# Kernel optimization log

Hardware: AMD Instinct MI355X
Metric: run time of the kernel (lower is better)

Reference implementation:

```python
import jax, jax.numpy as jnp
import numpy as np

TOP_K = 2


def setup_inputs() -> dict:
    key = jax.random.key(0)
    ks = jax.random.split(key, 6)
    B, S, D, E = 4, 2048, 1024, 8
    d_ff = 4 * D
    x = jax.random.normal(ks[0], (B, S, D), dtype=jnp.float32)
    router_w = jax.random.normal(ks[1], (E, D), dtype=jnp.float32) * 0.02
    w_fc = jax.random.normal(ks[2], (E, d_ff, D), dtype=jnp.float32) * 0.02
    w_proj = jax.random.normal(ks[3], (E, D, d_ff), dtype=jnp.float32) * 0.02
    shared_fc = jax.random.normal(ks[4], (d_ff, D), dtype=jnp.float32) * 0.02
    shared_proj = jax.random.normal(ks[5], (D, d_ff), dtype=jnp.float32) * 0.02
    return {"x": x, "router_w": router_w, "w_fc": w_fc, "w_proj": w_proj,
            "shared_fc": shared_fc, "shared_proj": shared_proj}


def _mlp(x, w_fc, w_proj):
    # c_proj(relu(c_fc(x))^2); torch Linear: y = x @ W.T
    return jnp.square(jax.nn.relu(x @ w_fc.T)) @ w_proj.T


def reference(x, router_w, w_fc, w_proj, shared_fc, shared_proj):
    B, S, D = x.shape
    E = router_w.shape[0]
    T = B * S
    flat = x.reshape(T, D)
    # Router: softmax in fp32, top-k, renormalize
    logits = flat @ router_w.T                                   # [T, E]
    probs = jax.nn.softmax(logits.astype(jnp.float32), axis=-1)
    topk_p, topk_i = jax.lax.top_k(probs, TOP_K)                 # [T, k]
    topk_w = (topk_p / jnp.maximum(topk_p.sum(-1, keepdims=True), 1e-9)).astype(flat.dtype)
    # Dense combine weights [T, E]: scatter normalized top-k weights per token
    combine = jnp.zeros((T, E), dtype=flat.dtype)
    combine = combine.at[jnp.arange(T)[:, None], topk_i].add(topk_w)
    # Expert compute (loop over small fixed E), weighted combine
    out = jnp.zeros_like(flat)
    for e in range(E):
        out = out + _mlp(flat, w_fc[e], w_proj[e]) * combine[:, e:e + 1]
    # Shared expert applied to all tokens
    out = out + _mlp(flat, shared_fc, shared_proj)
    return out.reshape(B, S, D)
```

## Files before the change

kernel.cpp:

```cpp
#include <hip/hip_runtime.h>

#define DEVFN __device__ __forceinline__

typedef _Float16 f16x8 __attribute__((ext_vector_type(8)));
typedef float f32x4 __attribute__((ext_vector_type(4)));

static constexpr int T   = 8192;
static constexpr int D   = 1024;
static constexpr int E   = 8;
static constexpr int DFF = 4096;
static constexpr int NG  = E + 1;
static constexpr int RTOT = 3*T;
static constexpr int MAXRT = (2*T)/128 + E + T/128;

DEVFN unsigned short f2h_bits(float v){
  _Float16 h = (_Float16)v;
  return __builtin_bit_cast(unsigned short, h);
}

DEVFN void gload_lds16(const void* g, void* l){
  __builtin_amdgcn_global_load_lds((const __attribute__((address_space(1))) void*)g,
                                   (__attribute__((address_space(3))) void*)l, 16, 0, 0);
}

__global__ __launch_bounds__(256) void cast_all_kernel(
    const float* __restrict__ s0, const float* __restrict__ s1,
    const float* __restrict__ s2, const float* __restrict__ s3,
    unsigned short* __restrict__ d0, unsigned short* __restrict__ d1,
    unsigned short* __restrict__ d2, unsigned short* __restrict__ d3,
    int n0, int n1, int n2, int n3){
  int total = n0 + n1 + n2 + n3;
  for (int j = blockIdx.x*256 + threadIdx.x; j < total; j += gridDim.x*256){
    const float* sp; unsigned short* dp; int loc = j;
    if (loc < n0){ sp = s0; dp = d0; }
    else if ((loc -= n0) < n1){ sp = s1; dp = d1; }
    else if ((loc -= n1) < n2){ sp = s2; dp = d2; }
    else { loc -= n2; sp = s3; dp = d3; }
    float4 v = ((const float4*)sp)[loc];
    ushort4 o;
    o.x = f2h_bits(v.x); o.y = f2h_bits(v.y); o.z = f2h_bits(v.z); o.w = f2h_bits(v.w);
    ((ushort4*)dp)[loc] = o;
  }
}

__global__ __launch_bounds__(256) void router_kernel(const float* __restrict__ x,
    const float* __restrict__ rw, unsigned short* __restrict__ xb,
    int* __restrict__ tok_e, float* __restrict__ tok_w, int* __restrict__ counts){
  const int lane = threadIdx.x & 63;
  const int t = blockIdx.x*4 + (threadIdx.x >> 6);
  const float4* xp = (const float4*)(x + (size_t)t*D);
  ushort4* xo = (ushort4*)(xb + (size_t)t*D);
  float acc[E];
#pragma unroll
  for (int e=0;e<E;e++) acc[e]=0.f;
#pragma unroll
  for (int i=0;i<4;i++){
    float4 xv = xp[lane + (i<<6)];
    ushort4 o; o.x=f2h_bits(xv.x); o.y=f2h_bits(xv.y); o.z=f2h_bits(xv.z); o.w=f2h_bits(xv.w);
    xo[lane + (i<<6)] = o;
#pragma unroll
    for (int e=0;e<E;e++){
      float4 wv = ((const float4*)(rw + e*D))[lane + (i<<6)];
      acc[e] = fmaf(xv.x,wv.x, fmaf(xv.y,wv.y, fmaf(xv.z,wv.z, fmaf(xv.w,wv.w, acc[e]))));
    }
  }
#pragma unroll
  for (int e=0;e<E;e++){
#pragma unroll
    for (int off=32; off>0; off>>=1) acc[e] += __shfl_xor(acc[e], off);
  }
  if (lane==0){
    float l0=-1e30f, l1=-1e30f; int e0=0, e1=0;
#pragma unroll
    for (int e=0;e<E;e++){
      float v = acc[e];
      if (v > l0){ l1=l0; e1=e0; l0=v; e0=e; }
      else if (v > l1){ l1=v; e1=e; }
    }
    float r   = expf(l1 - l0);
    float inv = 1.f/(1.f + r);
    tok_e[2*t]   = e0; tok_e[2*t+1] = e1;
    tok_w[2*t]   = inv; tok_w[2*t+1] = r*inv;
    atomicAdd(&counts[e0], 1);
    atomicAdd(&counts[e1], 1);
  }
}

__global__ void scan_kernel(const int* __restrict__ counts, int* __restrict__ offs,
                            int* __restrict__ tile_g, int* __restrict__ tile_r0,
                            int* __restrict__ nrt){
  if (blockIdx.x==0 && threadIdx.x==0){
    int off=0, nt=0;
    for (int e=0;e<E;e++){
      offs[e]=off;
      int c = counts[e];
      int tiles = (c+127)>>7;
      for (int i=0;i<tiles;i++){ tile_g[nt]=e; tile_r0[nt]=off + (i<<7); nt++; }
      off += c;
    }
    offs[E] = off;
    for (int i=0;i<T/128;i++){ tile_g[nt]=E; tile_r0[nt]=2*T + (i<<7); nt++; }
    offs[E+1] = 3*T;
    *nrt = nt;
  }
}

__global__ __launch_bounds__(256) void scatter_kernel(const int* __restrict__ tok_e,
    const float* __restrict__ tok_w, const int* __restrict__ offs,
    int* __restrict__ fill, int* __restrict__ row_tok, float* __restrict__ row_w,
    int* __restrict__ inv2){
  int idx = blockIdx.x*256 + threadIdx.x;
  if (idx < 2*T){
    int e = tok_e[idx];
    int pos = offs[e] + atomicAdd(&fill[e], 1);
    row_tok[pos] = idx >> 1;
    row_w[pos]   = tok_w[idx];
    inv2[idx]    = pos;
  } else {
    row_tok[idx] = idx - 2*T;
    row_w[idx]   = 1.0f;
  }
}

template<int MODE>
__global__ __launch_bounds__(256, 2) void gemm8p_kernel(
    const unsigned short* __restrict__ A, const unsigned short* __restrict__ Ball,
    unsigned short* __restrict__ O,
    const int K, const int N, const int CT,
    const int* __restrict__ tile_g, const int* __restrict__ tile_r0,
    const int* __restrict__ offs, const int* __restrict__ nrt,
    const int* __restrict__ row_tok)
{
  const int nwg  = gridDim.x * gridDim.y;
  const int orig = blockIdx.y * gridDim.x + blockIdx.x;
  const int q8 = nwg >> 3, r8 = nwg & 7;
  const int xcd = orig & 7, pos = orig >> 3;
  const int wg = (xcd < r8 ? xcd*(q8+1) : r8*(q8+1) + (xcd-r8)*q8) + pos;
  const int rt = wg / CT, ct = wg - rt*CT;
  if (rt >= *nrt) return;

  const int g    = tile_g[rt];
  const int row0 = tile_r0[rt];
  const int row_end = offs[g+1];
  const unsigned short* Bp = Ball + (size_t)g * (size_t)N * (size_t)K;

  __shared__ __align__(16) unsigned short As[2*2*4096];
  __shared__ __align__(16) unsigned short Bs[2*2*4096];

  const int tid  = threadIdx.x;
  const int lane = tid & 63;
  const int wave = tid >> 6;

  const unsigned short* aS[2];
  const unsigned short* bS[2];
  int ldst[2];
#pragma unroll
  for (int c=0;c<2;c++){
    int s  = (c<<8) + tid;
    int rr = s >> 2;
    int qg = (s & 3) ^ ((rr >> 1) & 3);
    int ar;
    if constexpr (MODE==0){
      int grow = row0 + rr;
      if (grow > row_end-1) grow = row_end-1;
      ar = row_tok[grow];
    } else {
      ar = row0 + rr;
    }
    aS[c] = A  + (size_t)ar*K + qg*8;
    bS[c] = Bp + (size_t)((ct<<7) + rr)*K + qg*8;
    ldst[c] = ((c<<8) + (wave<<6))*8;
  }

#define STAGE_A(KT,KS) { _Pragma("unroll") for (int c=0;c<2;c++) \
    gload_lds16(aS[c] + (KT)*64 + (KS)*32, As + ((((KT)&1)*2+(KS))<<12) + ldst[c]); }
#define STAGE_B(KT,KS) { _Pragma("unroll") for (int c=0;c<2;c++) \
    gload_lds16(bS[c] + (KT)*64 + (KS)*32, Bs + ((((KT)&1)*2+(KS))<<12) + ldst[c]); }

  const int wm = wave >> 1, wn = wave & 1;
  const int q16g = lane >> 4;
  int aoff[4], boff[4];
#pragma unroll
  for (int m=0;m<4;m++){
    int r = (wm<<6) + (m<<4) + (lane&15);
    aoff[m] = (r<<5) + ((q16g ^ ((r>>1)&3))<<3);
  }
#pragma unroll
  for (int n=0;n<4;n++){
    int r = (wn<<6) + (n<<4) + (lane&15);
    boff[n] = (r<<5) + ((q16g ^ ((r>>1)&3))<<3);
  }

#define BARS { __builtin_amdgcn_s_barrier(); __builtin_amdgcn_sched_barrier(0); }
#define VMW(NN) asm volatile("s_waitcnt vmcnt(" #NN ")" ::: "memory");
#define DSA(BUF,KS) { const unsigned short* hb = As + (((BUF)*2+(KS))<<12); \
    _Pragma("unroll") for (int m=0;m<4;m++) af[m] = *(const f16x8*)(hb + aoff[m]); }
#define DSB(BUF,KS) { const unsigned short* hb = Bs + (((BUF)*2+(KS))<<12); \
    _Pragma("unroll") for (int n=0;n<4;n++) bf[n] = *(const f16x8*)(hb + boff[n]); }
#define MFMA16 { __builtin_amdgcn_s_setprio(1); \
    _Pragma("unroll") for (int m=0;m<4;m++) \
    _Pragma("unroll") for (int n=0;n<4;n++) \
      acc[m][n] = __builtin_amdgcn_mfma_f32_16x16x32_f16(af[m], bf[n], acc[m][n], 0, 0, 0); \
    __builtin_amdgcn_s_setprio(0); }

  f32x4 acc[4][4] = {};
  const int nkt = K >> 6;

  STAGE_A(0,0); STAGE_B(0,0); STAGE_A(0,1); STAGE_B(0,1);
  VMW(4); BARS;

  f16x8 af[4], bf[4];
  for (int t=0; t<nkt; ++t){
    const int buf = t & 1;
    const bool more = (t+1 < nkt);
    DSA(buf,0); DSB(buf,0);
    if (more) { STAGE_A(t+1,0); STAGE_B(t+1,0); VMW(4); }
    else      { VMW(0); }
    BARS; MFMA16; BARS;
    DSA(buf,1); DSB(buf,1);
    if (more) { STAGE_A(t+1,1); STAGE_B(t+1,1); VMW(4); }
    BARS; MFMA16;
    if (more) BARS;
  }

  const int lcol = lane & 15;
  const int lrow = (lane >> 4) << 2;
#pragma unroll
  for (int m=0;m<4;m++){
#pragma unroll
    for (int q=0;q<4;q++){
      const int grow = row0 + (wm<<6) + (m<<4) + lrow + q;
      if (grow >= row_end) continue;
#pragma unroll
      for (int n=0;n<4;n++){
        const int col = (ct<<7) + (wn<<6) + (n<<4) + lcol;
        float v = acc[m][n][q];
        if constexpr (MODE==0) v = (v > 0.f) ? v*v : 0.f;
        O[(size_t)grow*N + col] = f2h_bits(v);
      }
    }
  }
#undef STAGE_A
#undef STAGE_B
#undef BARS
#undef VMW
#undef DSA
#undef DSB
#undef MFMA16
}

__global__ __launch_bounds__(256) void combine_kernel(const unsigned short* __restrict__ y,
    const int* __restrict__ inv2, const float* __restrict__ row_w, float* __restrict__ out){
  int gid = blockIdx.x*256 + threadIdx.x;
  int t = gid >> 7, c = gid & 127;
  int p0 = inv2[2*t], p1 = inv2[2*t+1];
  float w0 = row_w[p0], w1 = row_w[p1];
  f16x8 v0 = *(const f16x8*)(y + (size_t)p0*D      + c*8);
  f16x8 v1 = *(const f16x8*)(y + (size_t)p1*D      + c*8);
  f16x8 v2 = *(const f16x8*)(y + (size_t)(2*T+t)*D + c*8);
  float4 o0, o1;
  float r[8];
#pragma unroll
  for (int j=0;j<8;j++)
    r[j] = fmaf(w0, (float)v0[j], fmaf(w1, (float)v1[j], (float)v2[j]));
  o0.x=r[0]; o0.y=r[1]; o0.z=r[2]; o0.w=r[3];
  o1.x=r[4]; o1.y=r[5]; o1.z=r[6]; o1.w=r[7];
  float4* op = (float4*)(out + (size_t)t*D + c*8);
  op[0] = o0; op[1] = o1;
}

extern "C" void kernel_launch(void* const* d_in, const int* in_sizes, int n_in,
                              void* d_out, int out_size, void* d_ws, size_t ws_size,
                              hipStream_t stream){
  const float* x     = (const float*)d_in[0];
  const float* rw    = (const float*)d_in[1];
  const float* wfc   = (const float*)d_in[2];
  const float* wproj = (const float*)d_in[3];
  const float* sfc   = (const float*)d_in[4];
  const float* sproj = (const float*)d_in[5];
  float* out = (float*)d_out;

  char* ws = (char*)d_ws;
  size_t off = 0;
  auto alloc = [&](size_t bytes)->void*{
    void* p = ws + off; off += (bytes + 255) & ~(size_t)255; return p;
  };
  unsigned short* xb    = (unsigned short*)alloc((size_t)T*D*2);
  unsigned short* wall  = (unsigned short*)alloc((size_t)NG*DFF*D*2);
  unsigned short* wpall = (unsigned short*)alloc((size_t)NG*D*DFF*2);
  unsigned short* h     = (unsigned short*)alloc((size_t)RTOT*DFF*2);
  int*   tok_e   = (int*)  alloc((size_t)T*2*4);
  float* tok_w   = (float*)alloc((size_t)T*2*4);
  int*   row_tok = (int*)  alloc((size_t)RTOT*4);
  float* row_w   = (float*)alloc((size_t)RTOT*4);
  int*   inv2    = (int*)  alloc((size_t)2*T*4);
  int* counts  = (int*)alloc(E*4);
  int* fill    = (int*)alloc(E*4);
  int* offs    = (int*)alloc((E+2)*4);
  int* nrt     = (int*)alloc(4);
  int* tile_g  = (int*)alloc(MAXRT*4);
  int* tile_r0 = (int*)alloc(MAXRT*4);
  if (off > ws_size) return;

  unsigned short* y = wall;

  hipMemsetAsync(counts, 0, E*4, stream);
  hipMemsetAsync(fill,   0, E*4, stream);

  cast_all_kernel<<<2048, 256, 0, stream>>>(
      wfc, sfc, wproj, sproj,
      wall, wall + (size_t)E*DFF*D, wpall, wpall + (size_t)E*D*DFF,
      E*DFF*D/4, DFF*D/4, E*D*DFF/4, D*DFF/4);

  router_kernel <<<T/4, 256, 0, stream>>>(x, rw, xb, tok_e, tok_w, counts);
  scan_kernel   <<<1,   64,  0, stream>>>(counts, offs, tile_g, tile_r0, nrt);
  scatter_kernel<<<RTOT/256, 256, 0, stream>>>(tok_e, tok_w, offs, fill, row_tok, row_w, inv2);

  gemm8p_kernel<0><<<dim3(DFF/128, MAXRT), 256, 0, stream>>>(
      xb, wall, h, D, DFF, DFF/128, tile_g, tile_r0, offs, nrt, row_tok);
  gemm8p_kernel<1><<<dim3(D/128, MAXRT), 256, 0, stream>>>(
      h, wpall, y, DFF, D, D/128, tile_g, tile_r0, offs, nrt, row_tok);
  combine_kernel<<<(T*128)/256, 256, 0, stream>>>(y, inv2, row_w, out);
}
```

Before: 968.0 us.

## Restructure GEMM main loop into 4-stage LDS ring with register double-buffering

```diff
diff --git a/kernel.cpp b/kernel.cpp
--- a/kernel.cpp
+++ b/kernel.cpp
@@ -123,7 +123,7 @@
 }
 
 template<int MODE>
-__global__ __launch_bounds__(256, 2) void gemm8p_kernel(
+DEVFN void gemm_core(
     const unsigned short* __restrict__ A, const unsigned short* __restrict__ Ball,
     unsigned short* __restrict__ O,
     const int K, const int N, const int CT,
@@ -144,8 +144,8 @@
   const int row_end = offs[g+1];
   const unsigned short* Bp = Ball + (size_t)g * (size_t)N * (size_t)K;
 
-  __shared__ __align__(16) unsigned short As[2*2*4096];
-  __shared__ __align__(16) unsigned short Bs[2*2*4096];
+  __shared__ __align__(16) unsigned short As[4*4096];
+  __shared__ __align__(16) unsigned short Bs[4*4096];
 
   const int tid  = threadIdx.x;
   const int lane = tid & 63;
@@ -156,9 +156,9 @@
   int ldst[2];
 #pragma unroll
   for (int c=0;c<2;c++){
-    int s  = (c<<8) + tid;
-    int rr = s >> 2;
-    int qg = (s & 3) ^ ((rr >> 1) & 3);
+    int s_lin = (c<<8) + tid;
+    int rr = s_lin >> 2;
+    int qg = (s_lin & 3) ^ ((rr >> 1) & 3);
     int ar;
     if constexpr (MODE==0){
       int grow = row0 + rr;
@@ -172,10 +172,11 @@
     ldst[c] = ((c<<8) + (wave<<6))*8;
   }
 
-#define STAGE_A(KT,KS) { _Pragma("unroll") for (int c=0;c<2;c++) \
-    gload_lds16(aS[c] + (KT)*64 + (KS)*32, As + ((((KT)&1)*2+(KS))<<12) + ldst[c]); }
-#define STAGE_B(KT,KS) { _Pragma("unroll") for (int c=0;c<2;c++) \
-    gload_lds16(bS[c] + (KT)*64 + (KS)*32, Bs + ((((KT)&1)*2+(KS))<<12) + ldst[c]); }
+#define STAGE(KT) { \
+    _Pragma("unroll") for (int c=0;c<2;c++) \
+      gload_lds16(aS[c] + (KT)*32, As + (((KT)&3)<<12) + ldst[c]); \
+    _Pragma("unroll") for (int c=0;c<2;c++) \
+      gload_lds16(bS[c] + (KT)*32, Bs + (((KT)&3)<<12) + ldst[c]); }
 
   const int wm = wave >> 1, wn = wave & 1;
   const int q16g = lane >> 4;
@@ -191,36 +192,40 @@
     boff[n] = (r<<5) + ((q16g ^ ((r>>1)&3))<<3);
   }
 
-#define BARS { __builtin_amdgcn_s_barrier(); __builtin_amdgcn_sched_barrier(0); }
+#define SB0 __builtin_amdgcn_sched_barrier(0);
+#define BAR __builtin_amdgcn_s_barrier();
 #define VMW(NN) asm volatile("s_waitcnt vmcnt(" #NN ")" ::: "memory");
-#define DSA(BUF,KS) { const unsigned short* hb = As + (((BUF)*2+(KS))<<12); \
-    _Pragma("unroll") for (int m=0;m<4;m++) af[m] = *(const f16x8*)(hb + aoff[m]); }
-#define DSB(BUF,KS) { const unsigned short* hb = Bs + (((BUF)*2+(KS))<<12); \
-    _Pragma("unroll") for (int n=0;n<4;n++) bf[n] = *(const f16x8*)(hb + boff[n]); }
-#define MFMA16 { __builtin_amdgcn_s_setprio(1); \
+#define READF(AX,BX,KT) { \
+    const unsigned short* pa = As + (((KT)&3)<<12); \
+    const unsigned short* pb = Bs + (((KT)&3)<<12); \
+    _Pragma("unroll") for (int m=0;m<4;m++) AX[m] = *(const f16x8*)(pa + aoff[m]); \
+    _Pragma("unroll") for (int n=0;n<4;n++) BX[n] = *(const f16x8*)(pb + boff[n]); }
+#define MFMA16(AX,BX) { __builtin_amdgcn_s_setprio(1); \
     _Pragma("unroll") for (int m=0;m<4;m++) \
     _Pragma("unroll") for (int n=0;n<4;n++) \
-      acc[m][n] = __builtin_amdgcn_mfma_f32_16x16x32_f16(af[m], bf[n], acc[m][n], 0, 0, 0); \
+      acc[m][n] = __builtin_amdgcn_mfma_f32_16x16x32_f16(AX[m], BX[n], acc[m][n], 0, 0, 0); \
     __builtin_amdgcn_s_setprio(0); }
+#define STEP(S, CA, CB, NA, NB) { \
+    if ((S)+1 < NS) READF(NA, NB, (S)+1); \
+    if ((S)+3 < NS) STAGE((S)+3); \
+    MFMA16(CA, CB); \
+    if ((S)+3 < NS) { VMW(4); } \
+    else if ((S)+2 < NS) { VMW(0); } \
+    if ((S)+1 < NS) { BAR; SB0; } }
 
   f32x4 acc[4][4] = {};
-  const int nkt = K >> 6;
-
-  STAGE_A(0,0); STAGE_B(0,0); STAGE_A(0,1); STAGE_B(0,1);
-  VMW(4); BARS;
-
-  f16x8 af[4], bf[4];
-  for (int t=0; t<nkt; ++t){
-    const int buf = t & 1;
-    const bool more = (t+1 < nkt);
-    DSA(buf,0); DSB(buf,0);
-    if (more) { STAGE_A(t+1,0); STAGE_B(t+1,0); VMW(4); }
-    else      { VMW(0); }
-    BARS; MFMA16; BARS;
-    DSA(buf,1); DSB(buf,1);
-    if (more) { STAGE_A(t+1,1); STAGE_B(t+1,1); VMW(4); }
-    BARS; MFMA16;
-    if (more) BARS;
+  const int NS = K >> 5;
+
+  STAGE(0); STAGE(1); STAGE(2);
+  VMW(4); BAR; SB0;
+
+  f16x8 aE[4], bE[4], aO[4], bO[4];
+  READF(aE, bE, 0);
+
+  for (int i=0;i<NS/2;++i){
+    const int s0 = 2*i;
+    STEP(s0,   aE, bE, aO, bO);
+    STEP(s0+1, aO, bO, aE, bE);
   }
 
   const int lcol = lane & 15;
@@ -240,13 +245,30 @@
       }
     }
   }
-#undef STAGE_A
-#undef STAGE_B
-#undef BARS
+#undef STAGE
+#undef SB0
+#undef BAR
 #undef VMW
-#undef DSA
-#undef DSB
+#undef READF
 #undef MFMA16
+#undef STEP
+}
+
+__global__ __launch_bounds__(256, 2) void gemm_fc(
+    const unsigned short* __restrict__ A, const unsigned short* __restrict__ Ball,
+    unsigned short* __restrict__ O, const int K, const int N, const int CT,
+    const int* __restrict__ tile_g, const int* __restrict__ tile_r0,
+    const int* __restrict__ offs, const int* __restrict__ nrt,
+    const int* __restrict__ row_tok){
+  gemm_core<0>(A, Ball, O, K, N, CT, tile_g, tile_r0, offs, nrt, row_tok);
+}
+__global__ __launch_bounds__(256, 2) void gemm_proj(
+    const unsigned short* __restrict__ A, const unsigned short* __restrict__ Ball,
+    unsigned short* __restrict__ O, const int K, const int N, const int CT,
+    const int* __restrict__ tile_g, const int* __restrict__ tile_r0,
+    const int* __restrict__ offs, const int* __restrict__ nrt,
+    const int* __restrict__ row_tok){
+  gemm_core<1>(A, Ball, O, K, N, CT, tile_g, tile_r0, offs, nrt, row_tok);
 }
 
 __global__ __launch_bounds__(256) void combine_kernel(const unsigned short* __restrict__ y,
@@ -316,9 +338,9 @@
   scan_kernel   <<<1,   64,  0, stream>>>(counts, offs, tile_g, tile_r0, nrt);
   scatter_kernel<<<RTOT/256, 256, 0, stream>>>(tok_e, tok_w, offs, fill, row_tok, row_w, inv2);
 
-  gemm8p_kernel<0><<<dim3(DFF/128, MAXRT), 256, 0, stream>>>(
+  gemm_fc  <<<dim3(DFF/128, MAXRT), 256, 0, stream>>>(
       xb, wall, h, D, DFF, DFF/128, tile_g, tile_r0, offs, nrt, row_tok);
-  gemm8p_kernel<1><<<dim3(D/128, MAXRT), 256, 0, stream>>>(
+  gemm_proj<<<dim3(D/128, MAXRT), 256, 0, stream>>>(
       h, wpall, y, DFF, D, D/128, tile_g, tile_r0, offs, nrt, row_tok);
   combine_kernel<<<(T*128)/256, 256, 0, stream>>>(y, inv2, row_w, out);
 }
```

Measured after the change: 973.4 us (median of 2 runs). About the same (+0.6%).
